# Kernel optimization log

Hardware: AMD Instinct MI355X
Metric: run time of the kernel (lower is better)

Reference implementation:

```python
import jax, jax.numpy as jnp
import numpy as np

N_NODES = 50000
N_EDGES = 1_600_000
IN_DIM = 256
HIDDEN = 256
OUT_DIM = 48
K = 10
ALPHA = 0.5


def _ppr_temp(K, alpha):
    # PPR init from GPR_prop: temp[k] = alpha*(1-alpha)^k, temp[K] = (1-alpha)^K
    t = alpha * (1 - alpha) ** np.arange(K + 1, dtype=np.float32)
    t[-1] = (1 - alpha) ** K
    return jnp.asarray(t, dtype=jnp.float32)


def setup_inputs() -> dict:
    key = jax.random.key(0)
    ks = jax.random.split(key, 7)
    x = jax.random.normal(ks[0], (N_NODES, IN_DIM), dtype=jnp.float32)
    edge_index = jax.random.randint(ks[1], (2, N_EDGES), 0, N_NODES, dtype=jnp.int64)
    # Linear layers (torch Linear: y = x @ W.T + b); store as [in, out]
    lim1 = 1.0 / np.sqrt(IN_DIM)
    W1 = jax.random.uniform(ks[2], (IN_DIM, HIDDEN), jnp.float32, -lim1, lim1)
    b1 = jax.random.uniform(ks[3], (HIDDEN,), jnp.float32, -lim1, lim1)
    lim2 = 1.0 / np.sqrt(HIDDEN)
    W2 = jax.random.uniform(ks[4], (HIDDEN, OUT_DIM), jnp.float32, -lim2, lim2)
    b2 = jax.random.uniform(ks[5], (OUT_DIM,), jnp.float32, -lim2, lim2)
    temp = _ppr_temp(K, ALPHA)
    return {"x": x, "edge_index": edge_index, "W1": W1, "b1": b1,
            "W2": W2, "b2": b2, "temp": temp}


def reference(x, edge_index, W1, b1, W2, b2, temp):
    N = x.shape[0]
    # MLP head (dropout in eval mode -> identity)
    h = jax.nn.relu(x @ W1 + b1)
    h = h @ W2 + b2  # [N, OUT_DIM]

    # GCN normalization with self-loops: norm_e = deg^-1/2[src] * deg^-1/2[dst]
    loops = jnp.arange(N, dtype=edge_index.dtype)
    src = jnp.concatenate([edge_index[0], loops])
    dst = jnp.concatenate([edge_index[1], loops])
    deg = jnp.zeros((N,), dtype=h.dtype).at[dst].add(1.0)
    dinv = jax.lax.rsqrt(jnp.maximum(deg, 1e-12))
    norm = (dinv[src] * dinv[dst])[:, None]  # [E+N, 1]

    # K-hop propagation with learned gamma mixing
    def step(carry, gamma):
        hk, hidden = carry
        msg = norm * hk[src]                              # gather + scale
        hk = jax.ops.segment_sum(msg, dst, num_segments=N)  # scatter-add
        return (hk, hidden + gamma * hk), None

    (_, hidden), _ = jax.lax.scan(step, (h, temp[0] * h), temp[1:])
    return jax.nn.log_softmax(hidden, axis=1)
```

## Files before the change

### kernel.cpp

```cpp
#include <hip/hip_runtime.h>
#include <hip/hip_fp16.h>
#include <math.h>

#define BSH    9
#define BNODES 512
#define NBMAX  128
#define CAP2   24576
#define ECHUNK 6144

typedef short bf16x8 __attribute__((ext_vector_type(8)));
typedef float f32x4 __attribute__((ext_vector_type(4)));

__device__ __forceinline__ unsigned f2b(float f) {
    union { float f; unsigned u; } x; x.f = f;
    return (x.u + 0x7fffu + ((x.u >> 16) & 1u)) >> 16;
}


__global__ __launch_bounds__(256) void k_zero(int* __restrict__ p, int n) {
    int i = blockIdx.x * 256 + threadIdx.x;
    if (i < n) p[i] = 0;
}


__global__ __launch_bounds__(256) void k_castx(const float4* __restrict__ x, uint4* __restrict__ xb, int n8) {
    int i = blockIdx.x * 256 + threadIdx.x;
    if (i >= n8) return;
    float4 f0 = x[2 * i], f1 = x[2 * i + 1];
    uint4 o;
    o.x = f2b(f0.x) | (f2b(f0.y) << 16);
    o.y = f2b(f0.z) | (f2b(f0.w) << 16);
    o.z = f2b(f1.x) | (f2b(f1.y) << 16);
    o.w = f2b(f1.z) | (f2b(f1.w) << 16);
    xb[i] = o;
}

__global__ __launch_bounds__(256) void k_castw(const float* __restrict__ W1, const float* __restrict__ W2,
                                               unsigned short* __restrict__ w1t, unsigned short* __restrict__ w2t) {
    int i = blockIdx.x * 256 + threadIdx.x;
    if (i < 65536) {
        int n = i >> 8, k = i & 255;
        w1t[i] = (unsigned short)f2b(W1[k * 256 + n]);
    } else if (i < 65536 + 12288) {
        int j = i - 65536;
        int n = j >> 8, k = j & 255;
        w2t[j] = (unsigned short)f2b(W2[k * 48 + n]);
    }
}


__global__ __launch_bounds__(256) void k_bin(const int* __restrict__ src, const int* __restrict__ dst,
                                             int* __restrict__ bktcnt, unsigned* __restrict__ stage,
                                             int E, int NB) {
    __shared__ unsigned ecache[ECHUNK];
    __shared__ int lcnt[NBMAX], lbase[NBMAX], lcur[NBMAX];
    const int t = threadIdx.x;
    for (int i = t; i < NBMAX; i += 256) { lcnt[i] = 0; lcur[i] = 0; }
    const int e0 = blockIdx.x * ECHUNK;
    const int m = min(ECHUNK, E - e0);
    __syncthreads();
    for (int i = t; i < m; i += 256) {
        int s = src[e0 + i], d = dst[e0 + i];
        ecache[i] = ((unsigned)d << 16) | (unsigned)s;
        atomicAdd(&lcnt[d >> BSH], 1);
    }
    __syncthreads();
    if (t < NB) lbase[t] = lcnt[t] ? atomicAdd(&bktcnt[t], lcnt[t]) : 0;
    __syncthreads();
    for (int i = t; i < m; i += 256) {
        unsigned p = ecache[i];
        int b = (int)(p >> (16 + BSH));
        int pos = lbase[b] + atomicAdd(&lcur[b], 1);
        if (pos < CAP2) stage[(size_t)b * CAP2 + pos] = p;
    }
}


__global__ __launch_bounds__(512) void k_cnt(const unsigned* __restrict__ stage,
                                             const int* __restrict__ bktcnt,
                                             int* __restrict__ cnt,
                                             float* __restrict__ dinv, float* __restrict__ dinv2,
                                             float* __restrict__ sdeg, int N) {
    __shared__ int dcnt[BNODES];
    const int b = blockIdx.x, t = threadIdx.x;
    dcnt[t] = 0;
    __syncthreads();
    const int m = min(bktcnt[b], CAP2);
    const unsigned* st = stage + (size_t)b * CAP2;
    for (int i = t; i < m; i += 512)
        atomicAdd(&dcnt[(st[i] >> 16) & (BNODES - 1)], 1);
    __syncthreads();
    int node = b * BNODES + t;
    if (node <= N) {
        int c = dcnt[t];
        cnt[node] = c;
        float d = (float)c + 1.0f;
        float r = rsqrtf(d);
        dinv[node] = r;
        dinv2[node] = r * r;
        sdeg[node] = d * r;
    }
}


__global__ __launch_bounds__(256) void k_scan1(const int* __restrict__ cnt, int* __restrict__ rowptr,
                                               int* __restrict__ blk, int NT) {
    __shared__ int s[256];
    int t = threadIdx.x, i = blockIdx.x * 256 + t;
    int v = (i < NT) ? ((cnt[i] + 7) & ~7) : 0;
    s[t] = v; __syncthreads();
#pragma unroll
    for (int off = 1; off < 256; off <<= 1) {
        int x = (t >= off) ? s[t - off] : 0; __syncthreads();
        s[t] += x; __syncthreads();
    }
    if (i < NT) rowptr[i] = s[t] - v;
    if (t == 255) blk[blockIdx.x] = s[255];
}

__global__ __launch_bounds__(256) void k_scan2(int* __restrict__ blk, int nb) {
    __shared__ int s[256];
    int t = threadIdx.x;
    int v = (t < nb) ? blk[t] : 0;
    s[t] = v; __syncthreads();
#pragma unroll
    for (int off = 1; off < 256; off <<= 1) {
        int x = (t >= off) ? s[t - off] : 0; __syncthreads();
        s[t] += x; __syncthreads();
    }
    if (t < nb) blk[t] = s[t] - v;
}

__global__ __launch_bounds__(256) void k_scan3(int* __restrict__ rowptr, const int* __restrict__ blk, int NT) {
    int i = blockIdx.x * 256 + threadIdx.x;
    if (i < NT) rowptr[i] += blk[blockIdx.x];
}


__global__ __launch_bounds__(512) void k_place(const unsigned* __restrict__ stage,
                                               const int* __restrict__ bktcnt,
                                               const int* __restrict__ rowptr,
                                               unsigned short* __restrict__ csr, int N) {
    __shared__ int lcur[BNODES];
    const int b = blockIdx.x, t = threadIdx.x;
    const int node = b * BNODES + t;
    lcur[t] = (node < N) ? rowptr[node] : 0;
    __syncthreads();
    const int m = min(bktcnt[b], CAP2);
    const unsigned* st = stage + (size_t)b * CAP2;
    for (int i = t; i < m; i += 512) {
        unsigned p = st[i];
        int dl = (int)((p >> 16) & (BNODES - 1));
        int pos = atomicAdd(&lcur[dl], 1);
        csr[pos] = (unsigned short)(p & 0xffffu);
    }
    __syncthreads();
    if (node < N) {
        int e1 = rowptr[node + 1];
        for (int i = lcur[t]; i < e1; ++i) csr[i] = (unsigned short)N;
    }
}


__global__ __launch_bounds__(256) void k_mgemm1(const unsigned short* __restrict__ xb,
                                                const unsigned short* __restrict__ w1t,
                                                const float* __restrict__ bias,
                                                unsigned short* __restrict__ h1b, int M) {
    __shared__ unsigned short sbuf[128 * 136];
    unsigned short* As = sbuf;
    unsigned short* Bs = sbuf + 128 * 40;
    const int t = threadIdx.x;
    const int bm = blockIdx.x * 128;
    const int bn = blockIdx.y * 128;
    const int w = t >> 6, lane = t & 63;
    const int q = lane >> 4, l16 = lane & 15;

    f32x4 acc[2][8] = {};
    const int ar0 = t >> 2;
    const int kc  = t & 3;
    const int swz_st = ((kc ^ (ar0 & 3)) * 8);
    int gr0 = bm + ar0;       if (gr0 >= M) gr0 = M - 1;
    int gr1 = bm + ar0 + 64;  if (gr1 >= M) gr1 = M - 1;
    const int swz_rd = (q ^ (l16 & 3)) * 8;

    for (int k0 = 0; k0 < 256; k0 += 32) {
        uint4 a0 = *(const uint4*)&xb[(size_t)gr0 * 256 + k0 + kc * 8];
        uint4 a1 = *(const uint4*)&xb[(size_t)gr1 * 256 + k0 + kc * 8];
        uint4 b0 = *(const uint4*)&w1t[(size_t)(bn + ar0) * 256 + k0 + kc * 8];
        uint4 b1 = *(const uint4*)&w1t[(size_t)(bn + ar0 + 64) * 256 + k0 + kc * 8];
        __syncthreads();
        *(uint4*)&As[ar0 * 40 + swz_st] = a0;
        *(uint4*)&As[(ar0 + 64) * 40 + swz_st] = a1;
        *(uint4*)&Bs[ar0 * 40 + swz_st] = b0;
        *(uint4*)&Bs[(ar0 + 64) * 40 + swz_st] = b1;
        __syncthreads();
        bf16x8 af0 = *(bf16x8*)&As[(w * 32 + l16) * 40 + swz_rd];
        bf16x8 af1 = *(bf16x8*)&As[(w * 32 + 16 + l16) * 40 + swz_rd];
#pragma unroll
        for (int j = 0; j < 8; ++j) {
            bf16x8 bf = *(bf16x8*)&Bs[(j * 16 + l16) * 40 + swz_rd];
            acc[0][j] = __builtin_amdgcn_mfma_f32_16x16x32_bf16(af0, bf, acc[0][j], 0, 0, 0);
            acc[1][j] = __builtin_amdgcn_mfma_f32_16x16x32_bf16(af1, bf, acc[1][j], 0, 0, 0);
        }
    }
    __syncthreads();
#pragma unroll
    for (int j = 0; j < 8; ++j) {
        int col = j * 16 + l16;
        float bb = bias[bn + col];
#pragma unroll
        for (int i = 0; i < 2; ++i) {
#pragma unroll
            for (int r = 0; r < 4; ++r) {
                float v = fmaxf(acc[i][j][r] + bb, 0.f);
                sbuf[(w * 32 + i * 16 + q * 4 + r) * 136 + col] = (unsigned short)f2b(v);
            }
        }
    }
    __syncthreads();
    const int row = t >> 1;
    const int ch = (t & 1) * 64;
    if (bm + row < M) {
#pragma unroll
        for (int i = 0; i < 8; ++i) {
            uint4 v = *(uint4*)&sbuf[row * 136 + ch + i * 8];
            *(uint4*)&h1b[(size_t)(bm + row) * 256 + bn + ch + i * 8] = v;
        }
    }
}


__global__ __launch_bounds__(256) void k_mgemm2(const unsigned short* __restrict__ h1b,
                                                const unsigned short* __restrict__ w2t,
                                                const float* __restrict__ bias,
                                                const float* __restrict__ dinv,
                                                __half* __restrict__ u0, int M) {
    __shared__ unsigned short As[128 * 40];
    __shared__ unsigned short Bs[48 * 40];
    const int t = threadIdx.x;
    const int bm = blockIdx.x * 128;
    const int w = t >> 6, lane = t & 63;
    const int q = lane >> 4, l16 = lane & 15;

    f32x4 acc[2][3] = {};
    const int ar0 = t >> 2;
    const int kc  = t & 3;
    const int swz_st = ((kc ^ (ar0 & 3)) * 8);
    int gr0 = bm + ar0;      if (gr0 >= M) gr0 = M - 1;
    int gr1 = bm + ar0 + 64; if (gr1 >= M) gr1 = M - 1;
    const int swz_rd = (q ^ (l16 & 3)) * 8;

    for (int k0 = 0; k0 < 256; k0 += 32) {
        uint4 a0 = *(const uint4*)&h1b[(size_t)gr0 * 256 + k0 + kc * 8];
        uint4 a1 = *(const uint4*)&h1b[(size_t)gr1 * 256 + k0 + kc * 8];
        uint4 bv;
        if (t < 192) bv = *(const uint4*)&w2t[(size_t)ar0 * 256 + k0 + kc * 8];
        __syncthreads();
        *(uint4*)&As[ar0 * 40 + swz_st] = a0;
        *(uint4*)&As[(ar0 + 64) * 40 + swz_st] = a1;
        if (t < 192) *(uint4*)&Bs[ar0 * 40 + swz_st] = bv;
        __syncthreads();
        bf16x8 af0 = *(bf16x8*)&As[(w * 32 + l16) * 40 + swz_rd];
        bf16x8 af1 = *(bf16x8*)&As[(w * 32 + 16 + l16) * 40 + swz_rd];
#pragma unroll
        for (int j = 0; j < 3; ++j) {
            bf16x8 bf = *(bf16x8*)&Bs[(j * 16 + l16) * 40 + swz_rd];
            acc[0][j] = __builtin_amdgcn_mfma_f32_16x16x32_bf16(af0, bf, acc[0][j], 0, 0, 0);
            acc[1][j] = __builtin_amdgcn_mfma_f32_16x16x32_bf16(af1, bf, acc[1][j], 0, 0, 0);
        }
    }
#pragma unroll
    for (int j = 0; j < 3; ++j) {
        int col = j * 16 + l16;
        float bb = bias[col];
#pragma unroll
        for (int i = 0; i < 2; ++i) {
#pragma unroll
            for (int r = 0; r < 4; ++r) {
                int row = bm + w * 32 + i * 16 + q * 4 + r;
                if (row < M) {
                    float v = (acc[i][j][r] + bb) * dinv[row];
                    u0[(size_t)row * 64 + col] = __float2half(v);
                }
            }
        }
    }
}


__global__ __launch_bounds__(256) void k_hop(const __half* __restrict__ u, __half* __restrict__ unxt,
                                             const int* __restrict__ rowptr,
                                             const unsigned short* __restrict__ csr,
                                             const float* __restrict__ dinv2, int NT) {
    int n = blockIdx.x * 4 + (threadIdx.x >> 6);
    if (n >= NT) return;
    const int lane = threadIdx.x & 63;
    const int c = lane & 7;
    const int j = lane >> 3;

    float acc[8] = {0.f, 0.f, 0.f, 0.f, 0.f, 0.f, 0.f, 0.f};
    const int e0 = rowptr[n], e1 = rowptr[n + 1];
    int e = e0;
    for (; e + 32 <= e1; e += 32) {
        int sa = (int)csr[e + j];
        int sb = (int)csr[e + 8 + j];
        int sc = (int)csr[e + 16 + j];
        int sd = (int)csr[e + 24 + j];
        union { uint4 u4; __half2 h2[4]; } ga, gb, gc, gd;
        ga.u4 = *(const uint4*)(u + (size_t)sa * 64 + c * 8);
        gb.u4 = *(const uint4*)(u + (size_t)sb * 64 + c * 8);
        gc.u4 = *(const uint4*)(u + (size_t)sc * 64 + c * 8);
        gd.u4 = *(const uint4*)(u + (size_t)sd * 64 + c * 8);
#pragma unroll
        for (int i = 0; i < 4; ++i) {
            __half2 p = __hadd2(ga.h2[i], gb.h2[i]);
            __half2 qq = __hadd2(gc.h2[i], gd.h2[i]);
            float2 fp = __half22float2(p);
            float2 fq = __half22float2(qq);
            acc[2 * i]     += fp.x + fq.x;
            acc[2 * i + 1] += fp.y + fq.y;
        }
    }
    for (; e < e1; e += 8) {
        int sa = (int)csr[e + j];
        union { uint4 u4; __half2 h2[4]; } ga;
        ga.u4 = *(const uint4*)(u + (size_t)sa * 64 + c * 8);
#pragma unroll
        for (int i = 0; i < 4; ++i) {
            float2 fa = __half22float2(ga.h2[i]);
            acc[2 * i]     += fa.x;
            acc[2 * i + 1] += fa.y;
        }
    }
#pragma unroll
    for (int off = 8; off < 64; off <<= 1) {
#pragma unroll
        for (int i = 0; i < 8; ++i) acc[i] += __shfl_xor(acc[i], off);
    }
    if (j == 0 && c < 6) {
        union { uint4 u4; __half2 h2[4]; } sv, ov;
        sv.u4 = *(const uint4*)(u + (size_t)n * 64 + c * 8);
        float w2 = dinv2[n];
#pragma unroll
        for (int i = 0; i < 4; ++i) {
            float2 sf = __half22float2(sv.h2[i]);
            float2 r;
            r.x = (acc[2 * i]     + sf.x) * w2;
            r.y = (acc[2 * i + 1] + sf.y) * w2;
            ov.h2[i] = __float22half2_rn(r);
        }
        *(uint4*)(unxt + (size_t)n * 64 + c * 8) = ov.u4;
    }
}


__global__ __launch_bounds__(256) void k_final(const __half* __restrict__ u0, const __half* __restrict__ u1,
                                               size_t S, const float* __restrict__ sdeg,
                                               const float* __restrict__ temp,
                                               float* __restrict__ out, int N) {
    int w = (blockIdx.x * 256 + threadIdx.x) >> 6;
    int lane = threadIdx.x & 63;
    if (w >= N) return;
    size_t base = (size_t)w * 64 + lane;
    float val = 0.f, m = -INFINITY;
    if (lane < 48) {
        float acc = temp[0] * __half2float(u0[base]);
        const __half* uk = u1;
#pragma unroll
        for (int k = 1; k <= 10; ++k) {
            acc += temp[k] * __half2float(uk[base]);
            uk += S;
        }
        val = acc * sdeg[w];
        m = val;
    }
#pragma unroll
    for (int off = 32; off; off >>= 1) m = fmaxf(m, __shfl_xor(m, off));
    float ex = (lane < 48) ? __expf(val - m) : 0.f;
    float s = ex;
#pragma unroll
    for (int off = 32; off; off >>= 1) s += __shfl_xor(s, off);
    if (lane < 48) out[(size_t)w * 48 + lane] = val - m - __logf(s);
}


extern "C" void kernel_launch(void* const* d_in, const int* in_sizes, int n_in,
                              void* d_out, int out_size, void* d_ws, size_t ws_size,
                              hipStream_t stream) {
    const float* x    = (const float*)d_in[0];
    const int*   ei   = (const int*)d_in[1];
    const float* W1   = (const float*)d_in[2];
    const float* b1   = (const float*)d_in[3];
    const float* W2   = (const float*)d_in[4];
    const float* b2   = (const float*)d_in[5];
    const float* temp = (const float*)d_in[6];
    float* out = (float*)d_out;

    const int N = in_sizes[0] / 256;
    const int E = in_sizes[1] / 2;
    const int* src = ei;
    const int* dst = ei + E;

    const int NT  = N + 1;
    const int NT2 = N + 2;
    const int NB  = (NT + BNODES - 1) >> BSH;

    char* w8 = (char*)d_ws;
    size_t NP = (size_t)((NT2 + 63) & ~63);
    int*   cnt     = (int*)w8;
    int*   bktcnt  = cnt + NP;
    int*   rowptr  = bktcnt + 128;
    int*   blk     = rowptr + NP;
    float* dinv    = (float*)(blk + 256);
    float* dinv2   = dinv + NP;
    float* sdeg    = dinv2 + NP;
    unsigned short* csr = (unsigned short*)(sdeg + NP);
    size_t csr_i   = (((size_t)E + 32 * NT) / 2 + 32 + 63) & ~(size_t)63;
    unsigned short* w1t = (unsigned short*)((int*)(sdeg + NP) + csr_i);
    unsigned short* w2t = w1t + 65536;
    unsigned short* xb  = w2t + 12288 + 64;
    size_t S       = ((size_t)NT * 64 + 127) & ~(size_t)127;
    __half* u0     = (__half*)(xb + (size_t)N * 256);
    unsigned short* h1b = (unsigned short*)(u0 + S);
    unsigned* stage = (unsigned*)h1b;
    __half* u1     = (__half*)(h1b + (size_t)N * 256);

    const int nbS = (NT2 + 255) / 256;

    k_zero  <<<(int)((NP + 128 + 255) / 256), 256, 0, stream>>>(cnt, (int)(NP + 128));
    k_bin   <<<(E + ECHUNK - 1) / ECHUNK, 256, 0, stream>>>(src, dst, bktcnt, stage, E, NB);
    k_cnt   <<<NB, 512, 0, stream>>>(stage, bktcnt, cnt, dinv, dinv2, sdeg, N);
    k_scan1 <<<nbS, 256, 0, stream>>>(cnt, rowptr, blk, NT2);
    k_scan2 <<<1, 256, 0, stream>>>(blk, nbS);
    k_scan3 <<<nbS, 256, 0, stream>>>(rowptr, blk, NT2);
    k_place <<<NB, 512, 0, stream>>>(stage, bktcnt, rowptr, csr, N);

    k_castx <<<(N * 256 / 8 + 255) / 256, 256, 0, stream>>>((const float4*)x, (uint4*)xb, N * 256 / 8);
    k_castw <<<(65536 + 12288 + 255) / 256, 256, 0, stream>>>(W1, W2, w1t, w2t);

    dim3 g1((N + 127) / 128, 2);
    k_mgemm1<<<g1, 256, 0, stream>>>(xb, w1t, b1, h1b, N);
    k_mgemm2<<<(N + 127) / 128, 256, 0, stream>>>(h1b, w2t, b2, dinv, u0, N);
    k_zero  <<<1, 64, 0, stream>>>((int*)(u0 + (size_t)N * 64), 24);

    const int hopBlocks = (NT + 3) / 4;
    for (int k = 0; k < 10; ++k) {
        const __half* cur = (k == 0) ? u0 : (u1 + (size_t)(k - 1) * S);
        __half* nxt = u1 + (size_t)k * S;
        k_hop<<<hopBlocks, 256, 0, stream>>>(cur, nxt, rowptr, csr, dinv2, NT);
    }

    k_final<<<(N + 3) / 4, 256, 0, stream>>>(u0, u1, S, sdeg, temp, out, N);
}
```

Baseline: 461.7 us.

## Store later propagation hops in FP8 to halve gather traffic

The first two hops keep their fp16 feature storage. A transition kernel writes hop 3 as FP8, and hops 4 to 10 then gather and write 8-bit features using packed fp8 conversion intrinsics. The final mixing kernel reads the fp16 hops for the first terms and FP8 for the rest. This targets the memory-bound random gather bandwidth of the propagation, at the cost of much lower precision in the later hops. That precision loss may be acceptable because those hops carry small PPR weights.

```diff
diff --git a/kernel.cpp b/kernel.cpp
--- a/kernel.cpp
+++ b/kernel.cpp
@@ -288,10 +288,10 @@
 }
 
 
-__global__ __launch_bounds__(256) void k_hop(const __half* __restrict__ u, __half* __restrict__ unxt,
-                                             const int* __restrict__ rowptr,
-                                             const unsigned short* __restrict__ csr,
-                                             const float* __restrict__ dinv2, int NT) {
+__global__ __launch_bounds__(256) void k_hop16(const __half* __restrict__ u, __half* __restrict__ unxt,
+                                               const int* __restrict__ rowptr,
+                                               const unsigned short* __restrict__ csr,
+                                               const float* __restrict__ dinv2, int NT) {
     int n = blockIdx.x * 4 + (threadIdx.x >> 6);
     if (n >= NT) return;
     const int lane = threadIdx.x & 63;
@@ -354,22 +354,176 @@
 }
 
 
-__global__ __launch_bounds__(256) void k_final(const __half* __restrict__ u0, const __half* __restrict__ u1,
-                                               size_t S, const float* __restrict__ sdeg,
+__global__ __launch_bounds__(256) void k_hopm(const __half* __restrict__ u, unsigned char* __restrict__ un8,
+                                              const int* __restrict__ rowptr,
+                                              const unsigned short* __restrict__ csr,
+                                              const float* __restrict__ dinv2, int NT) {
+    int n = blockIdx.x * 4 + (threadIdx.x >> 6);
+    if (n >= NT) return;
+    const int lane = threadIdx.x & 63;
+    const int c = lane & 7;
+    const int j = lane >> 3;
+
+    float acc[8] = {0.f, 0.f, 0.f, 0.f, 0.f, 0.f, 0.f, 0.f};
+    const int e0 = rowptr[n], e1 = rowptr[n + 1];
+    int e = e0;
+    for (; e + 32 <= e1; e += 32) {
+        int sa = (int)csr[e + j];
+        int sb = (int)csr[e + 8 + j];
+        int sc = (int)csr[e + 16 + j];
+        int sd = (int)csr[e + 24 + j];
+        union { uint4 u4; __half2 h2[4]; } ga, gb, gc, gd;
+        ga.u4 = *(const uint4*)(u + (size_t)sa * 64 + c * 8);
+        gb.u4 = *(const uint4*)(u + (size_t)sb * 64 + c * 8);
+        gc.u4 = *(const uint4*)(u + (size_t)sc * 64 + c * 8);
+        gd.u4 = *(const uint4*)(u + (size_t)sd * 64 + c * 8);
+#pragma unroll
+        for (int i = 0; i < 4; ++i) {
+            __half2 p = __hadd2(ga.h2[i], gb.h2[i]);
+            __half2 qq = __hadd2(gc.h2[i], gd.h2[i]);
+            float2 fp = __half22float2(p);
+            float2 fq = __half22float2(qq);
+            acc[2 * i]     += fp.x + fq.x;
+            acc[2 * i + 1] += fp.y + fq.y;
+        }
+    }
+    for (; e < e1; e += 8) {
+        int sa = (int)csr[e + j];
+        union { uint4 u4; __half2 h2[4]; } ga;
+        ga.u4 = *(const uint4*)(u + (size_t)sa * 64 + c * 8);
+#pragma unroll
+        for (int i = 0; i < 4; ++i) {
+            float2 fa = __half22float2(ga.h2[i]);
+            acc[2 * i]     += fa.x;
+            acc[2 * i + 1] += fa.y;
+        }
+    }
+#pragma unroll
+    for (int off = 8; off < 64; off <<= 1) {
+#pragma unroll
+        for (int i = 0; i < 8; ++i) acc[i] += __shfl_xor(acc[i], off);
+    }
+    if (j == 0) {
+        unsigned w0 = 0u, w1 = 0u;
+        if (c < 6) {
+            union { uint4 u4; __half2 h2[4]; } sv;
+            sv.u4 = *(const uint4*)(u + (size_t)n * 64 + c * 8);
+            float w2 = dinv2[n];
+            float r0, r1, r2, r3, r4, r5, r6, r7;
+            {
+                float2 s0 = __half22float2(sv.h2[0]);
+                float2 s1 = __half22float2(sv.h2[1]);
+                float2 s2 = __half22float2(sv.h2[2]);
+                float2 s3 = __half22float2(sv.h2[3]);
+                r0 = (acc[0] + s0.x) * w2;  r1 = (acc[1] + s0.y) * w2;
+                r2 = (acc[2] + s1.x) * w2;  r3 = (acc[3] + s1.y) * w2;
+                r4 = (acc[4] + s2.x) * w2;  r5 = (acc[5] + s2.y) * w2;
+                r6 = (acc[6] + s3.x) * w2;  r7 = (acc[7] + s3.y) * w2;
+            }
+            w0 = (unsigned)__builtin_amdgcn_cvt_pk_fp8_f32(r0, r1, 0, false);
+            w0 = (unsigned)__builtin_amdgcn_cvt_pk_fp8_f32(r2, r3, (int)w0, true);
+            w1 = (unsigned)__builtin_amdgcn_cvt_pk_fp8_f32(r4, r5, 0, false);
+            w1 = (unsigned)__builtin_amdgcn_cvt_pk_fp8_f32(r6, r7, (int)w1, true);
+        }
+        *(uint2*)(un8 + (size_t)n * 64 + c * 8) = make_uint2(w0, w1);
+    }
+}
+
+
+__global__ __launch_bounds__(256) void k_hop8(const unsigned char* __restrict__ u8,
+                                              unsigned char* __restrict__ un8,
+                                              const int* __restrict__ rowptr,
+                                              const unsigned short* __restrict__ csr,
+                                              const float* __restrict__ dinv2, int NT, int N) {
+    int n = blockIdx.x * 4 + (threadIdx.x >> 6);
+    if (n >= NT) return;
+    const int lane = threadIdx.x & 63;
+    const int c = lane & 3;
+    const int j = lane >> 2;
+
+    float acc[16] = {0.f, 0.f, 0.f, 0.f, 0.f, 0.f, 0.f, 0.f,
+                     0.f, 0.f, 0.f, 0.f, 0.f, 0.f, 0.f, 0.f};
+    const int e0 = rowptr[n], e1 = rowptr[n + 1];
+#define ACC4(B, W) do { unsigned _w = (W); \
+    acc[B+0] += __builtin_amdgcn_cvt_f32_fp8((int)_w, 0); \
+    acc[B+1] += __builtin_amdgcn_cvt_f32_fp8((int)_w, 1); \
+    acc[B+2] += __builtin_amdgcn_cvt_f32_fp8((int)_w, 2); \
+    acc[B+3] += __builtin_amdgcn_cvt_f32_fp8((int)_w, 3); } while (0)
+    for (int e = e0; e < e1; e += 64) {
+        const int rem = e1 - e;
+        int s0 = (j < rem)      ? (int)csr[e + j]      : N;
+        int s1 = (16 + j < rem) ? (int)csr[e + 16 + j] : N;
+        int s2 = (32 + j < rem) ? (int)csr[e + 32 + j] : N;
+        int s3 = (48 + j < rem) ? (int)csr[e + 48 + j] : N;
+        uint4 g0 = *(const uint4*)(u8 + (size_t)s0 * 64 + c * 16);
+        uint4 g1 = *(const uint4*)(u8 + (size_t)s1 * 64 + c * 16);
+        uint4 g2 = *(const uint4*)(u8 + (size_t)s2 * 64 + c * 16);
+        uint4 g3 = *(const uint4*)(u8 + (size_t)s3 * 64 + c * 16);
+        ACC4(0, g0.x); ACC4(4, g0.y); ACC4(8, g0.z); ACC4(12, g0.w);
+        ACC4(0, g1.x); ACC4(4, g1.y); ACC4(8, g1.z); ACC4(12, g1.w);
+        ACC4(0, g2.x); ACC4(4, g2.y); ACC4(8, g2.z); ACC4(12, g2.w);
+        ACC4(0, g3.x); ACC4(4, g3.y); ACC4(8, g3.z); ACC4(12, g3.w);
+    }
+#undef ACC4
+#pragma unroll
+    for (int off = 4; off < 64; off <<= 1) {
+#pragma unroll
+        for (int i = 0; i < 16; ++i) acc[i] += __shfl_xor(acc[i], off);
+    }
+    if (lane < 4) {
+        uint4 o = make_uint4(0u, 0u, 0u, 0u);
+        if (lane < 3) {
+            uint4 sv = *(const uint4*)(u8 + (size_t)n * 64 + lane * 16);
+            float w2 = dinv2[n];
+            float r0  = (acc[0]  + __builtin_amdgcn_cvt_f32_fp8((int)sv.x, 0)) * w2;
+            float r1  = (acc[1]  + __builtin_amdgcn_cvt_f32_fp8((int)sv.x, 1)) * w2;
+            float r2  = (acc[2]  + __builtin_amdgcn_cvt_f32_fp8((int)sv.x, 2)) * w2;
+            float r3  = (acc[3]  + __builtin_amdgcn_cvt_f32_fp8((int)sv.x, 3)) * w2;
+            float r4  = (acc[4]  + __builtin_amdgcn_cvt_f32_fp8((int)sv.y, 0)) * w2;
+            float r5  = (acc[5]  + __builtin_amdgcn_cvt_f32_fp8((int)sv.y, 1)) * w2;
+            float r6  = (acc[6]  + __builtin_amdgcn_cvt_f32_fp8((int)sv.y, 2)) * w2;
+            float r7  = (acc[7]  + __builtin_amdgcn_cvt_f32_fp8((int)sv.y, 3)) * w2;
+            float r8  = (acc[8]  + __builtin_amdgcn_cvt_f32_fp8((int)sv.z, 0)) * w2;
+            float r9  = (acc[9]  + __builtin_amdgcn_cvt_f32_fp8((int)sv.z, 1)) * w2;
+            float r10 = (acc[10] + __builtin_amdgcn_cvt_f32_fp8((int)sv.z, 2)) * w2;
+            float r11 = (acc[11] + __builtin_amdgcn_cvt_f32_fp8((int)sv.z, 3)) * w2;
+            float r12 = (acc[12] + __builtin_amdgcn_cvt_f32_fp8((int)sv.w, 0)) * w2;
+            float r13 = (acc[13] + __builtin_amdgcn_cvt_f32_fp8((int)sv.w, 1)) * w2;
+            float r14 = (acc[14] + __builtin_amdgcn_cvt_f32_fp8((int)sv.w, 2)) * w2;
+            float r15 = (acc[15] + __builtin_amdgcn_cvt_f32_fp8((int)sv.w, 3)) * w2;
+            o.x = (unsigned)__builtin_amdgcn_cvt_pk_fp8_f32(r0,  r1,  0, false);
+            o.x = (unsigned)__builtin_amdgcn_cvt_pk_fp8_f32(r2,  r3,  (int)o.x, true);
+            o.y = (unsigned)__builtin_amdgcn_cvt_pk_fp8_f32(r4,  r5,  0, false);
+            o.y = (unsigned)__builtin_amdgcn_cvt_pk_fp8_f32(r6,  r7,  (int)o.y, true);
+            o.z = (unsigned)__builtin_amdgcn_cvt_pk_fp8_f32(r8,  r9,  0, false);
+            o.z = (unsigned)__builtin_amdgcn_cvt_pk_fp8_f32(r10, r11, (int)o.z, true);
+            o.w = (unsigned)__builtin_amdgcn_cvt_pk_fp8_f32(r12, r13, 0, false);
+            o.w = (unsigned)__builtin_amdgcn_cvt_pk_fp8_f32(r14, r15, (int)o.w, true);
+        }
+        *(uint4*)(un8 + (size_t)n * 64 + lane * 16) = o;
+    }
+}
+
+
+__global__ __launch_bounds__(256) void k_final(const __half* __restrict__ u0, size_t S16,
+                                               const unsigned char* __restrict__ w3, size_t S8B,
+                                               const float* __restrict__ sdeg,
                                                const float* __restrict__ temp,
                                                float* __restrict__ out, int N) {
     int w = (blockIdx.x * 256 + threadIdx.x) >> 6;
     int lane = threadIdx.x & 63;
     if (w >= N) return;
-    size_t base = (size_t)w * 64 + lane;
     float val = 0.f, m = -INFINITY;
     if (lane < 48) {
+        size_t base = (size_t)w * 64 + lane;
         float acc = temp[0] * __half2float(u0[base]);
-        const __half* uk = u1;
-#pragma unroll
-        for (int k = 1; k <= 10; ++k) {
-            acc += temp[k] * __half2float(uk[base]);
-            uk += S;
+        acc += temp[1] * __half2float(u0[base + S16]);
+        acc += temp[2] * __half2float(u0[base + 2 * S16]);
+        const unsigned char* p = w3 + (size_t)w * 64 + lane;
+#pragma unroll
+        for (int k = 3; k <= 10; ++k) {
+            acc += temp[k] * __builtin_amdgcn_cvt_f32_fp8((int)*p, 0);
+            p += S8B;
         }
         val = acc * sdeg[w];
         m = val;
@@ -419,11 +573,12 @@
     unsigned short* w1t = (unsigned short*)((int*)(sdeg + NP) + csr_i);
     unsigned short* w2t = w1t + 65536;
     unsigned short* xb  = w2t + 12288 + 64;
-    size_t S       = ((size_t)NT * 64 + 127) & ~(size_t)127;
+    size_t S16     = ((size_t)NT * 64 + 127) & ~(size_t)127;
     __half* u0     = (__half*)(xb + (size_t)N * 256);
-    unsigned short* h1b = (unsigned short*)(u0 + S);
+    unsigned short* h1b = (unsigned short*)(u0 + 3 * S16);
     unsigned* stage = (unsigned*)h1b;
-    __half* u1     = (__half*)(h1b + (size_t)N * 256);
+    size_t S8B     = ((size_t)NT * 64 + 255) & ~(size_t)255;
+    unsigned char* w3 = (unsigned char*)(h1b + (size_t)N * 256);
 
     const int nbS = (NT2 + 255) / 256;
 
@@ -444,11 +599,12 @@
     k_zero  <<<1, 64, 0, stream>>>((int*)(u0 + (size_t)N * 64), 24);
 
     const int hopBlocks = (NT + 3) / 4;
-    for (int k = 0; k < 10; ++k) {
-        const __half* cur = (k == 0) ? u0 : (u1 + (size_t)(k - 1) * S);
-        __half* nxt = u1 + (size_t)k * S;
-        k_hop<<<hopBlocks, 256, 0, stream>>>(cur, nxt, rowptr, csr, dinv2, NT);
-    }
-
-    k_final<<<(N + 3) / 4, 256, 0, stream>>>(u0, u1, S, sdeg, temp, out, N);
-}
+    k_hop16<<<hopBlocks, 256, 0, stream>>>(u0, u0 + S16, rowptr, csr, dinv2, NT);
+    k_hop16<<<hopBlocks, 256, 0, stream>>>(u0 + S16, u0 + 2 * S16, rowptr, csr, dinv2, NT);
+    k_hopm <<<hopBlocks, 256, 0, stream>>>(u0 + 2 * S16, w3, rowptr, csr, dinv2, NT);
+    for (int k = 4; k <= 10; ++k)
+        k_hop8<<<hopBlocks, 256, 0, stream>>>(w3 + (size_t)(k - 4) * S8B, w3 + (size_t)(k - 3) * S8B,
+                                              rowptr, csr, dinv2, NT, N);
+
+    k_final<<<(N + 3) / 4, 256, 0, stream>>>(u0, S16, w3, S8B, sdeg, temp, out, N);
+}
```

Result: slower. 541.1 us (+17.2%).
